# Kernel tuning notes

Hardware: AMD Instinct MI355X
Metric: run time of the kernel (lower is better)

Reference implementation:

```python
import jax, jax.numpy as jnp
import numpy as np

OUT_H, OUT_W = 32, 256  # hardcoded output grid in the original call()


def setup_inputs() -> dict:
    key = jax.random.key(0)
    k1, k2 = jax.random.split(key)
    img = jax.random.uniform(k1, (256, 512), dtype=jnp.float32)
    # fractional offset guarantees (i+pos0-ii)^2 + (j+pos1-ij)^2 > 0 everywhere
    pos = jax.random.uniform(k2, (2,), dtype=jnp.float32) * 8.0 + 0.3
    return {"img": img, "pos": pos}


def reference(img, pos):
    # r[i, j] = sum_{ii, ij} img[ii, ij] / ((i + pos0 - ii)^2 + (j + pos1 - ij)^2)
    H, W = img.shape
    ii = jnp.arange(H, dtype=img.dtype)
    ij = jnp.arange(W, dtype=img.dtype)
    j = jnp.arange(OUT_W, dtype=img.dtype)
    dy2 = (j[:, None] + pos[1] - ij[None, :]) ** 2  # [OUT_W, W]

    def row(carry, i):
        dx2 = (i + pos[0] - ii) ** 2                       # [H]
        w = 1.0 / (dx2[None, :, None] + dy2[:, None, :])   # [OUT_W, H, W]
        r_i = jnp.einsum('jhw,hw->j', w, img)              # [OUT_W]
        return carry, r_i

    i_vals = jnp.arange(OUT_H, dtype=img.dtype)
    _, r = jax.lax.scan(row, 0, i_vals)  # scan over 32 output rows keeps peak memory ~134 MB
    return r  # [OUT_H, OUT_W]
```

## Files before the change

kernel.cpp:

```cpp
#include <hip/hip_runtime.h>


typedef _Float16 half8 __attribute__((ext_vector_type(8)));
typedef float f32x4 __attribute__((ext_vector_type(4)));

constexpr int W = 512;
constexpr int NG = 36, JCN = 4, KCN = 4;
constexpr int GRID1 = NG * JCN * KCN;
constexpr int SB  = 216;
constexpr int PHB = SB * 2;
constexpr int UB  = 8 * PHB;
constexpr float KSCALE = 256.0f;

__global__ __launch_bounds__(256, 3) void corr_mfma(
    const float* __restrict__ img, const float* __restrict__ pos,
    float* __restrict__ ws)
{
    __shared__ __align__(16) _Float16 S[39 * 128];
    __shared__ __align__(16) _Float16 Kc[8 * 8 * SB];
    __shared__ __align__(16) float red[2048];

    const int tid = threadIdx.x;
    const int bid = blockIdx.x;
    const int kc = bid & 3, jc = (bid >> 2) & 3, g = bid >> 4;
    const int k0 = kc * 128, j0 = jc * 64;
    const int u0 = -255 + 8 * g;

    const float p0 = pos[0], p1 = pos[1];
    const int amax = j0 - k0 + 63;

    for (int z = tid; z < 2048; z += 256) red[z] = 0.0f;

    const int R0 = -u0 - 7;
    for (int un = tid; un < 39 * 16; un += 256) {
        const int rr = un >> 4, sg = un & 15;
        const int irow = R0 + rr;
        float4 f0 = make_float4(0.f, 0.f, 0.f, 0.f), f1 = f0;
        if (0 <= irow && irow < 256) {
            const float4* gp = (const float4*)(img + irow * W + k0 + sg * 8);
            f0 = gp[0]; f1 = gp[1];
        }
        half8 hv;
        hv[0] = (_Float16)f0.x; hv[1] = (_Float16)f0.y;
        hv[2] = (_Float16)f0.z; hv[3] = (_Float16)f0.w;
        hv[4] = (_Float16)f1.x; hv[5] = (_Float16)f1.y;
        hv[6] = (_Float16)f1.z; hv[7] = (_Float16)f1.w;
        const int c = (sg * 16) ^ ((rr & 7) << 4);
        *(half8*)((char*)S + rr * 256 + c) = hv;
    }

    for (int z = tid; z < 8 * 8 * SB; z += 256) {
        const int u  = z / (8 * SB);
        const int r2 = z - u * (8 * SB);
        const int p  = r2 / SB;
        const int s  = r2 - p * SB;
        const float dxu = (float)(u0 + u) + p0;
        const float dx2 = dxu * dxu;
        const float dy  = (float)(amax - s - p) + p1;
        Kc[z] = (_Float16)(KSCALE * __builtin_amdgcn_rcpf(dx2 + dy * dy));
    }
    __syncthreads();

    const int lane = tid & 63;
    const int wv = tid >> 6;
    const int m = lane & 15, hq = lane >> 4;

    int boff[4];
#pragma unroll
    for (int nt = 0; nt < 4; ++nt) {
        const int t0 = 63 - 16 * nt - m + 32 * wv + 8 * hq;
        const int p = t0 & 7;
        boff[nt] = p * PHB + 2 * (t0 - p);
    }
    const int cA = 64 * wv + 16 * hq;

    f32x4 acc[2][4];
#pragma unroll
    for (int mt = 0; mt < 2; ++mt)
#pragma unroll
        for (int nt = 0; nt < 4; ++nt)
            acc[mt][nt] = (f32x4){0.f, 0.f, 0.f, 0.f};

#pragma unroll
    for (int d = 0; d < 8; ++d) {
        const int rr0 = m + 7 - d;
        const int rr1 = rr0 + 16;
        const half8 af0 = *(const half8*)((const char*)S + rr0 * 256 + (cA ^ ((rr0 & 7) << 4)));
        const half8 af1 = *(const half8*)((const char*)S + rr1 * 256 + (cA ^ ((rr1 & 7) << 4)));
        const char* kb = (const char*)Kc + d * UB;
#pragma unroll
        for (int nt = 0; nt < 4; ++nt) {
            const half8 b = *(const half8*)(kb + boff[nt]);
            acc[0][nt] = __builtin_amdgcn_mfma_f32_16x16x32_f16(af0, b, acc[0][nt], 0, 0, 0);
            acc[1][nt] = __builtin_amdgcn_mfma_f32_16x16x32_f16(af1, b, acc[1][nt], 0, 0, 0);
        }
    }

#pragma unroll
    for (int mt = 0; mt < 2; ++mt)
#pragma unroll
        for (int nt = 0; nt < 4; ++nt)
#pragma unroll
            for (int q = 0; q < 4; ++q)
                atomicAdd(&red[(16 * mt + hq * 4 + q) * 64 + 16 * nt + m],
                          acc[mt][nt][q]);
    __syncthreads();

    {
        f32x4* wp = (f32x4*)(ws + bid * 2048);
        const f32x4* rv = (const f32x4*)red;
        wp[tid * 2]     = rv[tid * 2];
        wp[tid * 2 + 1] = rv[tid * 2 + 1];
    }
}

__global__ __launch_bounds__(256) void corr_sum(const float* __restrict__ ws,
                                               float* __restrict__ out)
{
    const int o = blockIdx.x * 256 + threadIdx.x;
    const int i = o >> 8, j = o & 255;
    const int jc = j >> 6, jl = j & 63;
    const int cell = i * 64 + jl;
    float s0 = 0.f, s1 = 0.f, s2 = 0.f, s3 = 0.f;
#pragma unroll 4
    for (int g = 0; g < NG; ++g) {
        const float* b = ws + (size_t)((g * JCN + jc) * KCN) * 2048 + cell;
        s0 += b[0];
        s1 += b[2048];
        s2 += b[2 * 2048];
        s3 += b[3 * 2048];
    }
    out[o] = (s0 + s1 + s2 + s3) * (1.0f / KSCALE);
}

extern "C" void kernel_launch(void* const* d_in, const int* in_sizes, int n_in,
                              void* d_out, int out_size, void* d_ws, size_t ws_size,
                              hipStream_t stream) {
    const float* img = (const float*)d_in[0];
    const float* pos = (const float*)d_in[1];
    float* out = (float*)d_out;
    float* wsf = (float*)d_ws;

    corr_mfma<<<GRID1, 256, 0, stream>>>(img, pos, wsf);
    corr_sum<<<32, 256, 0, stream>>>(wsf, out);
}
```

Baseline: 105.4 us.

## Merge K-chunks into 512-thread blocks and replace reduction kernel with global atomics

Each block now covers the full 512-column input width with 8 waves instead of splitting it into four 128-column chunks. The kernel table grows from 216 to 560 entries per phase, and the block count drops from 576 to 144. The separate workspace-summing kernel is removed: blocks atomically add their scaled tile into the output, which is zeroed beforehand with a memset. This cuts a kernel launch and workspace traffic, but the grid now has fewer, larger blocks with more LDS each, which may lower occupancy. Float atomics also make the summation order nondeterministic.

```diff
diff --git a/kernel.cpp b/kernel.cpp
--- a/kernel.cpp
+++ b/kernel.cpp
@@ -5,39 +5,40 @@
 typedef float f32x4 __attribute__((ext_vector_type(4)));
 
 constexpr int W = 512;
-constexpr int NG = 36, JCN = 4, KCN = 4;
-constexpr int GRID1 = NG * JCN * KCN;
-constexpr int SB  = 216;
+constexpr int NG = 36;
+constexpr int JCN = 4;
+constexpr int GRID = NG * JCN;
+constexpr int SB  = 560;
 constexpr int PHB = SB * 2;
 constexpr int UB  = 8 * PHB;
 constexpr float KSCALE = 256.0f;
 
-__global__ __launch_bounds__(256, 3) void corr_mfma(
+__global__ __launch_bounds__(512) void corr_one(
     const float* __restrict__ img, const float* __restrict__ pos,
-    float* __restrict__ ws)
+    float* __restrict__ out)
 {
-    __shared__ __align__(16) _Float16 S[39 * 128];
+    __shared__ __align__(16) _Float16 S[39 * 512];
     __shared__ __align__(16) _Float16 Kc[8 * 8 * SB];
     __shared__ __align__(16) float red[2048];
 
     const int tid = threadIdx.x;
     const int bid = blockIdx.x;
-    const int kc = bid & 3, jc = (bid >> 2) & 3, g = bid >> 4;
-    const int k0 = kc * 128, j0 = jc * 64;
+    const int jc = bid & 3, g = bid >> 2;
+    const int j0 = jc * 64;
     const int u0 = -255 + 8 * g;
+    const int amax = j0 + 63;
 
     const float p0 = pos[0], p1 = pos[1];
-    const int amax = j0 - k0 + 63;
 
-    for (int z = tid; z < 2048; z += 256) red[z] = 0.0f;
+    for (int z = tid; z < 2048; z += 512) red[z] = 0.0f;
 
     const int R0 = -u0 - 7;
-    for (int un = tid; un < 39 * 16; un += 256) {
-        const int rr = un >> 4, sg = un & 15;
+    for (int un = tid; un < 39 * 64; un += 512) {
+        const int rr = un >> 6, sg = un & 63;
         const int irow = R0 + rr;
         float4 f0 = make_float4(0.f, 0.f, 0.f, 0.f), f1 = f0;
         if (0 <= irow && irow < 256) {
-            const float4* gp = (const float4*)(img + irow * W + k0 + sg * 8);
+            const float4* gp = (const float4*)(img + irow * W + sg * 8);
             f0 = gp[0]; f1 = gp[1];
         }
         half8 hv;
@@ -46,18 +47,17 @@
         hv[4] = (_Float16)f1.x; hv[5] = (_Float16)f1.y;
         hv[6] = (_Float16)f1.z; hv[7] = (_Float16)f1.w;
         const int c = (sg * 16) ^ ((rr & 7) << 4);
-        *(half8*)((char*)S + rr * 256 + c) = hv;
+        *(half8*)((char*)S + rr * 1024 + c) = hv;
     }
 
-    for (int z = tid; z < 8 * 8 * SB; z += 256) {
-        const int u  = z / (8 * SB);
-        const int r2 = z - u * (8 * SB);
-        const int p  = r2 / SB;
-        const int s  = r2 - p * SB;
+    for (int z = tid; z < 8 * 8 * SB; z += 512) {
+        const int u = z / (8 * SB);
+        const int r = z - u * (8 * SB);
+        const int p = r / SB;
+        const int s = r - p * SB;
         const float dxu = (float)(u0 + u) + p0;
-        const float dx2 = dxu * dxu;
         const float dy  = (float)(amax - s - p) + p1;
-        Kc[z] = (_Float16)(KSCALE * __builtin_amdgcn_rcpf(dx2 + dy * dy));
+        Kc[z] = (_Float16)(KSCALE * __builtin_amdgcn_rcpf(dxu * dxu + dy * dy));
     }
     __syncthreads();
 
@@ -65,14 +65,16 @@
     const int wv = tid >> 6;
     const int m = lane & 15, hq = lane >> 4;
 
-    int boff[4];
+    int boff[2][4];
 #pragma unroll
-    for (int nt = 0; nt < 4; ++nt) {
-        const int t0 = 63 - 16 * nt - m + 32 * wv + 8 * hq;
-        const int p = t0 & 7;
-        boff[nt] = p * PHB + 2 * (t0 - p);
-    }
-    const int cA = 64 * wv + 16 * hq;
+    for (int ks = 0; ks < 2; ++ks)
+#pragma unroll
+        for (int nt = 0; nt < 4; ++nt) {
+            const int t0 = 63 - 16 * nt - m + 64 * wv + 32 * ks + 8 * hq;
+            const int p = t0 & 7;
+            boff[ks][nt] = p * PHB + 2 * (t0 - p);
+        }
+    const int cA0 = 128 * wv + 16 * hq;
 
     f32x4 acc[2][4];
 #pragma unroll
@@ -83,16 +85,21 @@
 
 #pragma unroll
     for (int d = 0; d < 8; ++d) {
+        const char* kb = (const char*)Kc + d * UB;
         const int rr0 = m + 7 - d;
         const int rr1 = rr0 + 16;
-        const half8 af0 = *(const half8*)((const char*)S + rr0 * 256 + (cA ^ ((rr0 & 7) << 4)));
-        const half8 af1 = *(const half8*)((const char*)S + rr1 * 256 + (cA ^ ((rr1 & 7) << 4)));
-        const char* kb = (const char*)Kc + d * UB;
+        const int sw = (rr0 & 7) << 4;
 #pragma unroll
-        for (int nt = 0; nt < 4; ++nt) {
-            const half8 b = *(const half8*)(kb + boff[nt]);
-            acc[0][nt] = __builtin_amdgcn_mfma_f32_16x16x32_f16(af0, b, acc[0][nt], 0, 0, 0);
-            acc[1][nt] = __builtin_amdgcn_mfma_f32_16x16x32_f16(af1, b, acc[1][nt], 0, 0, 0);
+        for (int ks = 0; ks < 2; ++ks) {
+            const int cc = cA0 + 64 * ks;
+            const half8 a0 = *(const half8*)((const char*)S + rr0 * 1024 + (cc ^ sw));
+            const half8 a1 = *(const half8*)((const char*)S + rr1 * 1024 + (cc ^ sw));
+#pragma unroll
+            for (int nt = 0; nt < 4; ++nt) {
+                const half8 b = *(const half8*)(kb + boff[ks][nt]);
+                acc[0][nt] = __builtin_amdgcn_mfma_f32_16x16x32_f16(a0, b, acc[0][nt], 0, 0, 0);
+                acc[1][nt] = __builtin_amdgcn_mfma_f32_16x16x32_f16(a1, b, acc[1][nt], 0, 0, 0);
+            }
         }
     }
 
@@ -102,35 +109,16 @@
         for (int nt = 0; nt < 4; ++nt)
 #pragma unroll
             for (int q = 0; q < 4; ++q)
-                atomicAdd(&red[(16 * mt + hq * 4 + q) * 64 + 16 * nt + m],
+                atomicAdd(&red[(16 * mt + 4 * hq + q) * 64 + 16 * nt + m],
                           acc[mt][nt][q]);
     __syncthreads();
 
-    {
-        f32x4* wp = (f32x4*)(ws + bid * 2048);
-        const f32x4* rv = (const f32x4*)red;
-        wp[tid * 2]     = rv[tid * 2];
-        wp[tid * 2 + 1] = rv[tid * 2 + 1];
+#pragma unroll
+    for (int k = 0; k < 4; ++k) {
+        const int cell = tid + 512 * k;
+        const int i = cell >> 6, jl = cell & 63;
+        atomicAdd(&out[i * 256 + j0 + jl], red[cell] * (1.0f / KSCALE));
     }
-}
-
-__global__ __launch_bounds__(256) void corr_sum(const float* __restrict__ ws,
-                                               float* __restrict__ out)
-{
-    const int o = blockIdx.x * 256 + threadIdx.x;
-    const int i = o >> 8, j = o & 255;
-    const int jc = j >> 6, jl = j & 63;
-    const int cell = i * 64 + jl;
-    float s0 = 0.f, s1 = 0.f, s2 = 0.f, s3 = 0.f;
-#pragma unroll 4
-    for (int g = 0; g < NG; ++g) {
-        const float* b = ws + (size_t)((g * JCN + jc) * KCN) * 2048 + cell;
-        s0 += b[0];
-        s1 += b[2048];
-        s2 += b[2 * 2048];
-        s3 += b[3 * 2048];
-    }
-    out[o] = (s0 + s1 + s2 + s3) * (1.0f / KSCALE);
 }
 
 extern "C" void kernel_launch(void* const* d_in, const int* in_sizes, int n_in,
@@ -139,8 +127,7 @@
     const float* img = (const float*)d_in[0];
     const float* pos = (const float*)d_in[1];
     float* out = (float*)d_out;
-    float* wsf = (float*)d_ws;
 
-    corr_mfma<<<GRID1, 256, 0, stream>>>(img, pos, wsf);
-    corr_sum<<<32, 256, 0, stream>>>(wsf, out);
+    hipMemsetAsync(out, 0, (size_t)out_size * sizeof(float), stream);
+    corr_one<<<GRID, 512, 0, stream>>>(img, pos, out);
 }
```

Result: faster. 88.85 us (-15.7%).
